# Kernel optimization log

Hardware: AMD Instinct MI355X
Metric: run time of the kernel (lower is better)

The kernel has to match this reference:

```python
import jax, jax.numpy as jnp
import numpy as np

QP = 127.0          # 2**(8-1)-1, signed symmetric int8
MIN_RANGE = 1e-6


def _ste_round(x):
    # round_pass: forward round, straight-through gradient
    return x + jax.lax.stop_gradient(jnp.round(x) - x)


def _quant_per_tensor(x):
    # symmetric per-tensor: scale = max|x| / Qp (grad flows through max as in source)
    scale = jnp.maximum(jnp.max(jnp.abs(x)), MIN_RANGE) / QP
    return _ste_round(x / scale), scale


def _qlinear(x2d, w, b):
    # faithful to _quantize_global (prefix_token_num=None path):
    #   out = (x_q @ w_q.T + bias) * (s_w * s_x)
    xq, sx = _quant_per_tensor(x2d)
    wq, sw = _quant_per_tensor(w)
    out = jnp.matmul(xq, wq.T) + b[None, :]
    return out * (sw * sx)


def setup_inputs() -> dict:
    key = jax.random.key(0)
    k = jax.random.split(key, 5)
    B, N, D, H = 8, 1024, 1024, 4096
    return {
        "x": jax.random.normal(k[0], (B, N, D), dtype=jnp.float32),
        "w1": jax.random.normal(k[1], (H, D), dtype=jnp.float32) * 0.02,
        "b1": jax.random.normal(k[2], (H,), dtype=jnp.float32) * 0.02,
        "w2": jax.random.normal(k[3], (D, H), dtype=jnp.float32) * 0.02,
        "b2": jax.random.normal(k[4], (D,), dtype=jnp.float32) * 0.02,
    }


def reference(x, w1, b1, w2, b2):
    B, N, D = x.shape
    h = _qlinear(x.reshape(-1, D), w1, b1)          # [B*N, H]
    h = jax.nn.gelu(h, approximate=False)            # exact GELU (nn.GELU default)
    o = _qlinear(h, w2, b2)                          # [B*N, D]
    return o.reshape(B, N, -1)
```

## Files before the change

kernel.cpp:

```cpp
#include <hip/hip_runtime.h>
#include <hip/hip_fp16.h>
#include <cstdint>
#include <cmath>

#define QP    127.0f
#define MINR  1e-6f

#define MTOK 8192
#define DDIM 1024
#define HDIM 4096

typedef __attribute__((ext_vector_type(4))) int int32x4;
typedef __attribute__((ext_vector_type(8))) short short8;

__device__ __forceinline__ void gload16(const void* g, void* l) {
    __builtin_amdgcn_global_load_lds(
        (const __attribute__((address_space(1))) void*)g,
        (__attribute__((address_space(3))) void*)l, 16, 0, 0);
}

__global__ void zero_scales_kernel(float* g) {
    if (threadIdx.x < 4) g[threadIdx.x] = 0.0f;
}

__device__ __forceinline__ float wave_block_max(float m) {
    #pragma unroll
    for (int off = 32; off; off >>= 1) m = fmaxf(m, __shfl_down(m, off));
    __shared__ float sm[4];
    int lane = threadIdx.x & 63, w = threadIdx.x >> 6;
    if (lane == 0) sm[w] = m;
    __syncthreads();
    float bm = 0.0f;
    if (threadIdx.x == 0) bm = fmaxf(fmaxf(sm[0], sm[1]), fmaxf(sm[2], sm[3]));
    return bm;
}

__device__ __forceinline__ void absmax_range(const float4* in4, int n4, int bid, int nb,
                                             float* gout) {
    int tid = bid * blockDim.x + threadIdx.x;
    int stride = nb * blockDim.x;
    float m = 0.0f;
    for (int i = tid; i < n4; i += stride) {
        float4 v = in4[i];
        m = fmaxf(m, fmaxf(fmaxf(fabsf(v.x), fabsf(v.y)), fmaxf(fabsf(v.z), fabsf(v.w))));
    }
    float bm = wave_block_max(m);
    if (threadIdx.x == 0) atomicMax((int*)gout, __float_as_int(bm));
}

__global__ void absmax3_kernel(const float* __restrict__ x, const float* __restrict__ w1,
                               const float* __restrict__ w2, float* __restrict__ gmax) {
    int b = blockIdx.x;
    if (b < 1024)      absmax_range((const float4*)x,  MTOK * DDIM / 4, b,        1024, gmax + 0);
    else if (b < 1536) absmax_range((const float4*)w1, HDIM * DDIM / 4, b - 1024,  512, gmax + 1);
    else               absmax_range((const float4*)w2, DDIM * HDIM / 4, b - 1536,  512, gmax + 3);
}

__device__ __forceinline__ void quant_range(const float4* in4, int* out4, int n4,
                                            int bid, int nb, const float* gm) {
    const float s = fmaxf(*gm, MINR) / QP;
    int tid = bid * blockDim.x + threadIdx.x;
    int stride = nb * blockDim.x;
    for (int i = tid; i < n4; i += stride) {
        float4 v = in4[i];
        int q0 = ((int)rintf(v.x / s)) & 255;
        int q1 = ((int)rintf(v.y / s)) & 255;
        int q2 = ((int)rintf(v.z / s)) & 255;
        int q3 = ((int)rintf(v.w / s)) & 255;
        out4[i] = q0 | (q1 << 8) | (q2 << 16) | (q3 << 24);
    }
}

__global__ void quant3_kernel(const float* __restrict__ x, const float* __restrict__ w1,
                              const float* __restrict__ w2, int8_t* __restrict__ xq,
                              int8_t* __restrict__ w1q, int8_t* __restrict__ w2q,
                              const float* __restrict__ gmax) {
    int b = blockIdx.x;
    if (b < 2048)      quant_range((const float4*)x,  (int*)xq,  MTOK * DDIM / 4, b,        2048, gmax + 0);
    else if (b < 3072) quant_range((const float4*)w1, (int*)w1q, HDIM * DDIM / 4, b - 2048, 1024, gmax + 1);
    else               quant_range((const float4*)w2, (int*)w2q, DDIM * HDIM / 4, b - 3072, 1024, gmax + 3);
}

__global__ void quant_h_kernel(const __half* __restrict__ h, int8_t* __restrict__ hq,
                               const float* __restrict__ gm) {
    const float s = fmaxf(*gm, MINR) / QP;
    const short8* in8 = (const short8*)h;
    int2* out8 = (int2*)hq;
    const int n8 = MTOK * HDIM / 8;
    int tid = blockIdx.x * blockDim.x + threadIdx.x;
    int stride = gridDim.x * blockDim.x;
    for (int i = tid; i < n8; i += stride) {
        short8 v = in8[i];
        int q[8];
        #pragma unroll
        for (int j = 0; j < 8; ++j) {
            __half_raw r; r.x = (unsigned short)v[j];
            float f = __half2float(__half(r));
            q[j] = ((int)rintf(f / s)) & 255;
        }
        int2 o;
        o.x = q[0] | (q[1] << 8) | (q[2] << 16) | (q[3] << 24);
        o.y = q[4] | (q[5] << 8) | (q[6] << 16) | (q[7] << 24);
        out8[i] = o;
    }
}

template<int KD, int ND, bool GELU_EPI, typename OUTT>
__global__ __launch_bounds__(256, 2)
void gemm_i8_kernel(const int8_t* __restrict__ A, const int8_t* __restrict__ B,
                    const float* __restrict__ bias,
                    const float* __restrict__ gmA, const float* __restrict__ gmB,
                    OUTT* __restrict__ out, float* __restrict__ omax) {
    constexpr int NBC = ND / 128;
    __shared__ int8_t lA[128 * 128];
    __shared__ int8_t lB[128 * 128];
    const int t = threadIdx.x;
    const int lane = t & 63;
    const int w = t >> 6;
    const int wm = (w >> 1) * 64;
    const int wn = (w & 1) * 64;
    const int lr = lane & 15;
    const int lg = lane >> 4;

    const int chunk = gridDim.x >> 3;
    const int logical = (blockIdx.x & 7) * chunk + (blockIdx.x >> 3);
    const int bc = logical % NBC;
    const int br = logical / NBC;

    const int8_t* Ab = A + (size_t)br * 128 * KD;
    const int8_t* Bb = B + (size_t)bc * 128 * KD;

    int32x4 acc[4][4] = {};

    for (int kt = 0; kt < KD / 128; ++kt) {
        #pragma unroll
        for (int i = 0; i < 4; ++i) {
            int c = t + i * 256;
            int r = c >> 3;
            int sl = c & 7;
            int sc = ((sl ^ (r & 7)) << 4);
            gload16(Ab + (size_t)r * KD + kt * 128 + sc, &lA[c * 16]);
            gload16(Bb + (size_t)r * KD + kt * 128 + sc, &lB[c * 16]);
        }
        __syncthreads();

        #pragma unroll
        for (int kk = 0; kk < 2; ++kk) {
            int32x4 af[4], bf[4];
            #pragma unroll
            for (int m = 0; m < 4; ++m) {
                int r = wm + m * 16 + lr;
                int g = kk * 4 + lg;
                af[m] = *(const int32x4*)&lA[r * 128 + ((g ^ (r & 7)) << 4)];
            }
            #pragma unroll
            for (int n = 0; n < 4; ++n) {
                int r = wn + n * 16 + lr;
                int g = kk * 4 + lg;
                bf[n] = *(const int32x4*)&lB[r * 128 + ((g ^ (r & 7)) << 4)];
            }
            #pragma unroll
            for (int m = 0; m < 4; ++m)
                #pragma unroll
                for (int n = 0; n < 4; ++n)
                    acc[m][n] = __builtin_amdgcn_mfma_i32_16x16x64_i8(af[m], bf[n], acc[m][n], 0, 0, 0);
        }
        __syncthreads();
    }

    const float sA = fmaxf(*gmA, MINR) / QP;
    const float sB = fmaxf(*gmB, MINR) / QP;
    const float s = sB * sA;
    float lmax = 0.0f;
    #pragma unroll
    for (int m = 0; m < 4; ++m) {
        #pragma unroll
        for (int n = 0; n < 4; ++n) {
            #pragma unroll
            for (int r = 0; r < 4; ++r) {
                int row = br * 128 + wm + m * 16 + lg * 4 + r;
                int col = bc * 128 + wn + n * 16 + lr;
                float f = (float)acc[m][n][r] + bias[col];
                f *= s;
                if (GELU_EPI) {
                    float gg = f * (erff(f / 1.41421356237309504880f) + 1.0f) * 0.5f;
                    out[(size_t)row * ND + col] = (OUTT)gg;
                    lmax = fmaxf(lmax, fabsf(gg));
                } else {
                    out[(size_t)row * ND + col] = (OUTT)f;
                }
            }
        }
    }
    if (GELU_EPI) {
        #pragma unroll
        for (int off = 32; off; off >>= 1) lmax = fmaxf(lmax, __shfl_down(lmax, off));
        __shared__ float red[4];
        if (lane == 0) red[w] = lmax;
        __syncthreads();
        if (t == 0) {
            float bm = fmaxf(fmaxf(red[0], red[1]), fmaxf(red[2], red[3]));
            atomicMax((int*)omax, __float_as_int(bm));
        }
    }
}

extern "C" void kernel_launch(void* const* d_in, const int* in_sizes, int n_in,
                              void* d_out, int out_size, void* d_ws, size_t ws_size,
                              hipStream_t stream) {
    const float* x  = (const float*)d_in[0];
    const float* w1 = (const float*)d_in[1];
    const float* b1 = (const float*)d_in[2];
    const float* w2 = (const float*)d_in[3];
    const float* b2 = (const float*)d_in[4];
    float* out = (float*)d_out;

    uint8_t* ws = (uint8_t*)d_ws;
    float*  gmax = (float*)ws;
    int8_t* xq   = (int8_t*)(ws + 256);
    int8_t* w1q  = xq  + (size_t)MTOK * DDIM;
    int8_t* w2q  = w1q + (size_t)HDIM * DDIM;
    int8_t* hq   = w2q + (size_t)DDIM * HDIM;
    __half* h    = (__half*)(hq + (size_t)MTOK * HDIM);

    zero_scales_kernel<<<1, 64, 0, stream>>>(gmax);

    absmax3_kernel<<<2048, 256, 0, stream>>>(x, w1, w2, gmax);
    quant3_kernel<<<4096, 256, 0, stream>>>(x, w1, w2, xq, w1q, w2q, gmax);

    gemm_i8_kernel<DDIM, HDIM, true, __half>
        <<<2048, 256, 0, stream>>>(xq, w1q, b1, gmax + 0, gmax + 1, h, gmax + 2);

    quant_h_kernel<<<2048, 256, 0, stream>>>(h, hq, gmax + 2);

    gemm_i8_kernel<HDIM, DDIM, false, float>
        <<<512, 256, 0, stream>>>(hq, w2q, b2, gmax + 2, gmax + 3, out, nullptr);
}
```

Before: 193.0 us.

## Store quantized int8 operands in contiguous 128x128 tile-major layout

The quantization kernels now write int8 data in a blocked layout where each 128x128 tile is a contiguous 16KB chunk, and the GEMM loads tiles from these contiguous blocks instead of strided rows. The goal is more contiguous global reads for the LDS-direct loads and fewer DRAM pages touched per tile. In exchange, the quant kernels do scattered 16-byte or 8-byte writes and some extra index arithmetic.

```diff
diff --git a/kernel.cpp b/kernel.cpp
--- a/kernel.cpp
+++ b/kernel.cpp
@@ -56,18 +56,33 @@
     else               absmax_range((const float4*)w2, DDIM * HDIM / 4, b - 1536,  512, gmax + 3);
 }
 
-__device__ __forceinline__ void quant_range(const float4* in4, int* out4, int n4,
-                                            int bid, int nb, const float* gm) {
+__device__ __forceinline__ int pack4q(float4 v, float s) {
+    return (((int)rintf(v.x / s)) & 255) | ((((int)rintf(v.y / s)) & 255) << 8) |
+           ((((int)rintf(v.z / s)) & 255) << 16) | ((((int)rintf(v.w / s)) & 255) << 24);
+}
+
+template<int K>
+__device__ __forceinline__ void quant_pack_range(const float* __restrict__ in,
+                                                 int8_t* __restrict__ out, int R,
+                                                 int bid, int nb,
+                                                 const float* __restrict__ gm) {
     const float s = fmaxf(*gm, MINR) / QP;
+    const float4* in4 = (const float4*)in;
+    const int total = R * (K / 16);
     int tid = bid * blockDim.x + threadIdx.x;
     int stride = nb * blockDim.x;
-    for (int i = tid; i < n4; i += stride) {
-        float4 v = in4[i];
-        int q0 = ((int)rintf(v.x / s)) & 255;
-        int q1 = ((int)rintf(v.y / s)) & 255;
-        int q2 = ((int)rintf(v.z / s)) & 255;
-        int q3 = ((int)rintf(v.w / s)) & 255;
-        out4[i] = q0 | (q1 << 8) | (q2 << 16) | (q3 << 24);
+    for (int i = tid; i < total; i += stride) {
+        int ib = i << 4;
+        int r  = ib / K;
+        int k0 = ib & (K - 1);
+        int32x4 q;
+        q[0] = pack4q(in4[i * 4 + 0], s);
+        q[1] = pack4q(in4[i * 4 + 1], s);
+        q[2] = pack4q(in4[i * 4 + 2], s);
+        q[3] = pack4q(in4[i * 4 + 3], s);
+        size_t off = ((size_t)((r >> 7) * (K >> 7) + (k0 >> 7)) << 14)
+                   + ((r & 127) << 7) + (k0 & 127);
+        *(int32x4*)(out + off) = q;
     }
 }
 
@@ -76,16 +91,15 @@
                               int8_t* __restrict__ w1q, int8_t* __restrict__ w2q,
                               const float* __restrict__ gmax) {
     int b = blockIdx.x;
-    if (b < 2048)      quant_range((const float4*)x,  (int*)xq,  MTOK * DDIM / 4, b,        2048, gmax + 0);
-    else if (b < 3072) quant_range((const float4*)w1, (int*)w1q, HDIM * DDIM / 4, b - 2048, 1024, gmax + 1);
-    else               quant_range((const float4*)w2, (int*)w2q, DDIM * HDIM / 4, b - 3072, 1024, gmax + 3);
+    if (b < 2048)      quant_pack_range<DDIM>(x,  xq,  MTOK, b,        2048, gmax + 0);
+    else if (b < 3072) quant_pack_range<DDIM>(w1, w1q, HDIM, b - 2048, 1024, gmax + 1);
+    else               quant_pack_range<HDIM>(w2, w2q, DDIM, b - 3072, 1024, gmax + 3);
 }
 
 __global__ void quant_h_kernel(const __half* __restrict__ h, int8_t* __restrict__ hq,
                                const float* __restrict__ gm) {
     const float s = fmaxf(*gm, MINR) / QP;
     const short8* in8 = (const short8*)h;
-    int2* out8 = (int2*)hq;
     const int n8 = MTOK * HDIM / 8;
     int tid = blockIdx.x * blockDim.x + threadIdx.x;
     int stride = gridDim.x * blockDim.x;
@@ -101,7 +115,11 @@
         int2 o;
         o.x = q[0] | (q[1] << 8) | (q[2] << 16) | (q[3] << 24);
         o.y = q[4] | (q[5] << 8) | (q[6] << 16) | (q[7] << 24);
-        out8[i] = o;
+        int r  = i >> 9;
+        int k0 = (i & 511) << 3;
+        size_t off = ((size_t)((r >> 7) * (HDIM >> 7) + (k0 >> 7)) << 14)
+                   + ((r & 127) << 7) + (k0 & 127);
+        *(int2*)(hq + off) = o;
     }
 }
 
@@ -111,6 +129,7 @@
                     const float* __restrict__ bias,
                     const float* __restrict__ gmA, const float* __restrict__ gmB,
                     OUTT* __restrict__ out, float* __restrict__ omax) {
+    constexpr int KT = KD / 128;
     constexpr int NBC = ND / 128;
     __shared__ int8_t lA[128 * 128];
     __shared__ int8_t lB[128 * 128];
@@ -127,20 +146,20 @@
     const int bc = logical % NBC;
     const int br = logical / NBC;
 
-    const int8_t* Ab = A + (size_t)br * 128 * KD;
-    const int8_t* Bb = B + (size_t)bc * 128 * KD;
+    const int8_t* Ab = A + ((size_t)br * KT << 14);
+    const int8_t* Bb = B + ((size_t)bc * KT << 14);
 
     int32x4 acc[4][4] = {};
 
-    for (int kt = 0; kt < KD / 128; ++kt) {
+    for (int kt = 0; kt < KT; ++kt) {
         #pragma unroll
         for (int i = 0; i < 4; ++i) {
             int c = t + i * 256;
             int r = c >> 3;
             int sl = c & 7;
-            int sc = ((sl ^ (r & 7)) << 4);
-            gload16(Ab + (size_t)r * KD + kt * 128 + sc, &lA[c * 16]);
-            gload16(Bb + (size_t)r * KD + kt * 128 + sc, &lB[c * 16]);
+            int src = r * 128 + ((sl ^ (r & 7)) << 4);
+            gload16(Ab + ((size_t)kt << 14) + src, &lA[c * 16]);
+            gload16(Bb + ((size_t)kt << 14) + src, &lB[c * 16]);
         }
         __syncthreads();
 
```

After: 194.0 us. No clear change (+0.5%).
